# Kernel tuning notes

Measured on AMD Instinct MI355X. Metric: run time of the kernel, lower is better.

The kernel has to match this reference:

```python
import jax, jax.numpy as jnp
import numpy as np

B = 16384          # batch of graphs
N = 4              # nodes per graph (hardcoded in module)
F_IN = 4           # node features
F_E = 4            # edge features
CH = 128           # EdgeConditionedConv channels
HID = 256          # final Dense units (gnn hidden_dim)
OBS_DIM = 3 + N * F_IN + N * N + N * N * F_E  # 99


def _glorot(k, shape, fan):
    return jax.random.normal(k, shape, jnp.float32) * (1.0 / np.sqrt(fan))


def setup_inputs() -> dict:
    key = jax.random.key(0)
    ks = jax.random.split(key, 8)
    return {
        "observations": jax.random.normal(ks[0], (B, OBS_DIM), jnp.float32),
        # ECCConv filter-generating network: single Dense(F_E -> CH*F_IN)
        "W_fgn": _glorot(ks[1], (F_E, CH * F_IN), F_E),
        "b_fgn": jnp.zeros((CH * F_IN,), jnp.float32),
        # ECCConv root weight + bias
        "W_root": _glorot(ks[2], (F_IN, CH), F_IN),
        "b_conv": jnp.zeros((CH,), jnp.float32),
        # GlobalAttnSumPool attention vector
        "attn_kernel": _glorot(ks[3], (CH,), CH),
        # final Dense(tanh)
        "W_dense": _glorot(ks[4], (CH, HID), CH),
        "b_dense": jnp.zeros((HID,), jnp.float32),
    }


def reference(observations, W_fgn, b_fgn, W_root, b_conv, attn_kernel, W_dense, b_dense):
    Bn = observations.shape[0]
    obs = observations[:, 3:]
    X = obs[:, : N * F_IN].reshape(Bn, N, F_IN)                     # [B,N,F]
    A = obs[:, N * F_IN : N * F_IN + N * N].reshape(Bn, N, N)        # [B,N,N]
    E = obs[:, N * F_IN + N * N :].reshape(Bn, N, N, F_E)            # [B,N,N,Fe]

    # EdgeConditionedConv: per-edge filter generated from edge features,
    # reshaped to (B, N, N, CH, F_IN)  [channels-out first, as in spektral]
    K = (E @ W_fgn + b_fgn).reshape(Bn, N, N, CH, F_IN)
    # out[b,t,c] = sum_{s,f} A[b,t,s] * K[b,t,s,c,f] * X[b,s,f]  + root + bias
    msg = jnp.einsum('btscf,bts,bsf->btc', K, A, X)
    Xc = jax.nn.relu(msg + X @ W_root + b_conv)                      # [B,N,CH]

    # GlobalAttnSumPool: softmax over nodes of X @ a, weighted sum
    attn = jax.nn.softmax(jnp.einsum('bnc,c->bn', Xc, attn_kernel), axis=-1)
    pooled = jnp.einsum('bn,bnc->bc', attn, Xc)                      # [B,CH]

    return jnp.tanh(pooled @ W_dense + b_dense)                      # [B,HID]
```

## Files before the change

kernel.cpp:

```cpp
#include <hip/hip_runtime.h>

#define OBS_DIM 99
#define CH      128
#define HID     256
#define BPB     16

typedef short s8v __attribute__((ext_vector_type(8)));
typedef short s4v __attribute__((ext_vector_type(4)));
typedef float f4v __attribute__((ext_vector_type(4)));

__device__ __forceinline__ float ftanh(float x) {
    const float t = __expf(2.f * x);
    return 1.f - 2.f * __builtin_amdgcn_rcpf(t + 1.f);
}

__device__ __forceinline__ unsigned short f2bf(float f) {
    union { float f; unsigned u; } v; v.f = f;
    unsigned r = (v.u + 0x7fffu + ((v.u >> 16) & 1u)) >> 16;
    return (unsigned short)r;
}

__device__ __forceinline__ float bf2f(unsigned short u) {
    union { unsigned u; float f; } v; v.u = ((unsigned)u) << 16;
    return v.f;
}

__device__ __forceinline__ int kmap(int vb, int g, int j) {
    return vb ? (g * 4 + (j & 3) + 16 * (j >> 2)) : (g * 8 + j);
}

__device__ __forceinline__ float wbig_val(int k, int c, const float* Wf,
                                          const float* bf, const float* Wr,
                                          const float* bc) {
    if (k < 16) return Wf[(k >> 2) * 512 + c * 4 + (k & 3)];
    if (k < 20) return bf[c * 4 + (k - 16)];
    if (k < 24) return Wr[(k - 20) * CH + c];
    if (k == 24) return bc[c];
    return 0.f;
}

__global__ __launch_bounds__(256) void prepack(const float* __restrict__ W,
                                               const float* __restrict__ Wf,
                                               const float* __restrict__ bf,
                                               const float* __restrict__ Wr,
                                               const float* __restrict__ bc,
                                               unsigned short* __restrict__ ws) {
    const int gid = blockIdx.x * 256 + threadIdx.x;
    if (gid < 8192) {
        const int vb = gid >> 12, g = gid & 4095;
        const int tile = g >> 6, l = g & 63;
        const int kt = tile >> 4, nt = tile & 15;
        const int h = nt * 16 + (l & 15);
        unsigned short vh[8], vl[8];
        #pragma unroll
        for (int j = 0; j < 8; ++j) {
            const int k = kt * 32 + kmap(vb, l >> 4, j);
            const float wv = W[(size_t)k * HID + h];
            vh[j] = f2bf(wv);
            vl[j] = f2bf(wv - bf2f(vh[j]));
        }
        unsigned short* dh = ws + (size_t)vb * 65536 + (size_t)g * 8;
        *reinterpret_cast<s8v*>(dh)         = *reinterpret_cast<const s8v*>(vh);
        *reinterpret_cast<s8v*>(dh + 32768) = *reinterpret_cast<const s8v*>(vl);
    } else if (gid < 9216) {
        const int g2 = gid - 8192;
        const int vb = g2 >> 9, rest = g2 & 511;
        const int nt = rest >> 6, l = rest & 63;
        const int c = nt * 16 + (l & 15);
        unsigned short vh[8], vl[8];
        #pragma unroll
        for (int j = 0; j < 8; ++j) {
            const int k = kmap(vb, l >> 4, j);
            const float wv = wbig_val(k, c, Wf, bf, Wr, bc);
            vh[j] = f2bf(wv);
            vl[j] = f2bf(wv - bf2f(vh[j]));
        }
        unsigned short* dh = ws + 131072 + (size_t)vb * 8192 + (size_t)(nt * 64 + l) * 8;
        *reinterpret_cast<s8v*>(dh)        = *reinterpret_cast<const s8v*>(vh);
        *reinterpret_cast<s8v*>(dh + 4096) = *reinterpret_cast<const s8v*>(vl);
    }

    if (blockIdx.x == 0 && threadIdx.x < 64) {
        const int lane = threadIdx.x;
        const int g = lane >> 4;
        s8v ac, ab2, lab, ones;
        #pragma unroll
        for (int j = 0; j < 8; ++j) {
            ac[j]   = (short)f2bf((float)(kmap(0, g, j) + 1));
            ab2[j]  = (short)f2bf((float)(kmap(1, g, j) + 1));
            lab[j]  = (short)f2bf((float)(lane & 15));
            ones[j] = (short)0x3F80;
        }
        const f4v z = {0.f, 0.f, 0.f, 0.f};
        const f4v dcc = __builtin_amdgcn_mfma_f32_16x16x32_bf16(ac,  ac,  z, 0, 0, 0);
        const f4v dcb = __builtin_amdgcn_mfma_f32_16x16x32_bf16(ac,  ab2, z, 0, 0, 0);
        const f4v dbc = __builtin_amdgcn_mfma_f32_16x16x32_bf16(ab2, ac,  z, 0, 0, 0);
        const float EXP = 11440.f;
        int variant = 3;
        if      (__all(dcc[0] == EXP)) variant = 0;
        else if (__all(dcb[0] == EXP)) variant = 1;
        else if (__all(dbc[0] == EXP)) variant = 2;

        const f4v rowv = __builtin_amdgcn_mfma_f32_16x16x32_bf16(lab, ones, z, 0, 0, 0);
        const f4v colv = __builtin_amdgcn_mfma_f32_16x16x32_bf16(ones, lab, z, 0, 0, 0);
        int bi[4], hx[4];
        #pragma unroll
        for (int r = 0; r < 4; ++r) {
            int bv = (int)(rowv[r] * 0.03125f + 0.5f);
            int hv = (int)(colv[r] * 0.03125f + 0.5f);
            bi[r] = bv < 0 ? 0 : (bv > 15 ? 15 : bv);
            hx[r] = hv < 0 ? 0 : (hv > 15 ? 15 : hv);
        }
        bool gb = (bi[0] >> 2 == bi[1] >> 2) && (bi[1] >> 2 == bi[2] >> 2) &&
                  (bi[2] >> 2 == bi[3] >> 2);
        gb = gb && (((1 << (bi[0] & 3)) | (1 << (bi[1] & 3)) |
                     (1 << (bi[2] & 3)) | (1 << (bi[3] & 3))) == 0xF);
        gb = gb && (hx[0] == hx[1]) && (hx[1] == hx[2]) && (hx[2] == hx[3]);
        const int pk = bi[0] | (bi[1] << 4) | (bi[2] << 8) | (bi[3] << 12)
                     | (hx[0] << 16) | (hx[1] << 20) | (hx[2] << 24) | (hx[3] << 28);
        int bip = pk & 0xFFFF;
        bool same = true;
        #pragma unroll
        for (int st = 1; st < 16; st <<= 1)
            same = same && (bip == __shfl_xor(bip, st, 64));
        unsigned mset = 1u << hx[0];
        #pragma unroll
        for (int st = 1; st < 16; st <<= 1)
            mset |= (unsigned)__shfl_xor((int)mset, st, 64);
        gb = gb && same && (mset == 0xFFFFu);
        const int gb_all = __all(gb ? 1 : 0);

        int* pr = reinterpret_cast<int*>(ws + 147456);
        pr[lane] = pk;
        if (lane == 0) pr[64] = variant | (gb_all ? 16 : 0);
    }
}

__global__ __launch_bounds__(256, 4) void gnn_main(
    const float* __restrict__ obs,
    const float* __restrict__ W_fgn,
    const float* __restrict__ b_fgn,
    const float* __restrict__ W_root,
    const float* __restrict__ b_conv,
    const float* __restrict__ attn_k,
    const float* __restrict__ W_dense,
    const unsigned short* __restrict__ wb,
    const int* __restrict__ probe,
    const float* __restrict__ b_dense,
    float* __restrict__ out)
{
    __shared__ __align__(16) unsigned char smem[18944];
    auto feat_h  = reinterpret_cast<unsigned short (*)[40]>(smem);
    auto feat_l  = reinterpret_cast<unsigned short (*)[40]>(smem + 5120);
    auto part    = reinterpret_cast<float (*)[64]>(smem);
    auto attnl   = reinterpret_cast<float*>(smem + 1024);
    auto lobs    = reinterpret_cast<float (*)[96]>(smem + 10240);
    auto lpool_h = reinterpret_cast<unsigned short (*)[136]>(smem + 10240);
    auto lpool_l = reinterpret_cast<unsigned short (*)[136]>(smem + 14592);
    auto poolf   = reinterpret_cast<float (*)[136]>(smem + 10240);

    const int tid  = threadIdx.x;
    const int b0   = blockIdx.x * BPB;
    const int lane = tid & 63;
    const int w    = tid >> 6;

    int variant = 3, groupable = 0;
    int bi_r[4] = {0, 0, 0, 0}, hx_r[4] = {0, 0, 0, 0};
    if (probe) {
        const int pk   = probe[lane];
        const int meta = probe[64];
        variant   = meta & 7;
        groupable = (meta >> 4) & 1;
        #pragma unroll
        for (int r = 0; r < 4; ++r) {
            bi_r[r] = (pk >> (4 * r)) & 15;
            hx_r[r] = (pk >> (16 + 4 * r)) & 15;
        }
    }

    for (int i = tid; i < BPB * 96; i += 256) {
        const int bi = i / 96, col = i - bi * 96;
        lobs[bi][col] = obs[(size_t)(b0 + bi) * OBS_DIM + 3 + col];
    }
    __syncthreads();

    {
        const int bi = tid >> 4, t = (tid >> 2) & 3, e = tid & 3;
        const int row = bi * 4 + t;
        float m[4] = {0.f, 0.f, 0.f, 0.f};
        #pragma unroll
        for (int s = 0; s < 4; ++s) {
            const float ae = lobs[bi][16 + t * 4 + s] * lobs[bi][32 + (t * 4 + s) * 4 + e];
            #pragma unroll
            for (int f = 0; f < 4; ++f) m[f] = fmaf(ae, lobs[bi][s * 4 + f], m[f]);
        }
        #pragma unroll
        for (int f = 0; f < 4; ++f) {
            const unsigned short h = f2bf(m[f]);
            feat_h[row][e * 4 + f] = h;
            feat_l[row][e * 4 + f] = f2bf(m[f] - bf2f(h));
        }
    }
    if (tid < 64) {
        const int bi = tid >> 2, t = tid & 3, row = bi * 4 + t;
        #pragma unroll
        for (int f = 0; f < 4; ++f) {
            float ax = 0.f;
            #pragma unroll
            for (int s = 0; s < 4; ++s)
                ax = fmaf(lobs[bi][16 + t * 4 + s], lobs[bi][s * 4 + f], ax);
            const unsigned short h = f2bf(ax);
            feat_h[row][16 + f] = h;
            feat_l[row][16 + f] = f2bf(ax - bf2f(h));
        }
    } else if (tid < 128) {
        const int q = tid - 64;
        const int bi = q >> 2, t = q & 3, row = bi * 4 + t;
        #pragma unroll
        for (int f = 0; f < 4; ++f) {
            const float xv = lobs[bi][t * 4 + f];
            const unsigned short h = f2bf(xv);
            feat_h[row][20 + f] = h;
            feat_l[row][20 + f] = f2bf(xv - bf2f(h));
        }
        feat_h[row][24] = 0x3F80; feat_l[row][24] = 0;
        #pragma unroll
        for (int k = 25; k < 32; ++k) { feat_h[row][k] = 0; feat_l[row][k] = 0; }
    }
    __syncthreads();

    if (variant < 3 && groupable) {
        const int hx0 = hx_r[0];
        const int ib  = bi_r[0] >> 2;

        const s8v* B1h = reinterpret_cast<const s8v*>(wb + 131072 + (variant == 1 ? 8192 : 0));
        const s8v* B1l = B1h + 512;
        s8v bh1[2], bl1[2];
        float akv[2];
        #pragma unroll
        for (int ctl = 0; ctl < 2; ++ctl) {
            const int idx = (w * 2 + ctl) * 64 + lane;
            bh1[ctl] = B1h[idx]; bl1[ctl] = B1l[idx];
            akv[ctl] = attn_k[w * 32 + ctl * 16 + hx0];
        }

        float xc[4][2][4];
        float part16[16];
        #pragma unroll
        for (int i = 0; i < 16; ++i) part16[i] = 0.f;

        #pragma unroll
        for (int rt = 0; rt < 4; ++rt) {
            const int row = rt * 16 + (lane & 15);
            s8v ah, al;
            if (variant != 2) {
                ah = *reinterpret_cast<const s8v*>(&feat_h[row][(lane >> 4) * 8]);
                al = *reinterpret_cast<const s8v*>(&feat_l[row][(lane >> 4) * 8]);
            } else {
                const s4v h0 = *reinterpret_cast<const s4v*>(&feat_h[row][(lane >> 4) * 4]);
                const s4v h1 = *reinterpret_cast<const s4v*>(&feat_h[row][16 + (lane >> 4) * 4]);
                const s4v l0 = *reinterpret_cast<const s4v*>(&feat_l[row][(lane >> 4) * 4]);
                const s4v l1 = *reinterpret_cast<const s4v*>(&feat_l[row][16 + (lane >> 4) * 4]);
                ah = __builtin_shufflevector(h0, h1, 0, 1, 2, 3, 4, 5, 6, 7);
                al = __builtin_shufflevector(l0, l1, 0, 1, 2, 3, 4, 5, 6, 7);
            }
            #pragma unroll
            for (int ctl = 0; ctl < 2; ++ctl) {
                f4v acc = {0.f, 0.f, 0.f, 0.f};
                acc = __builtin_amdgcn_mfma_f32_16x16x32_bf16(al, bh1[ctl], acc, 0, 0, 0);
                acc = __builtin_amdgcn_mfma_f32_16x16x32_bf16(ah, bl1[ctl], acc, 0, 0, 0);
                acc = __builtin_amdgcn_mfma_f32_16x16x32_bf16(ah, bh1[ctl], acc, 0, 0, 0);
                #pragma unroll
                for (int r = 0; r < 4; ++r) {
                    const float v = fmaxf(acc[r], 0.f);
                    xc[rt][ctl][r] = v;
                    part16[rt * 4 + r] = fmaf(v, akv[ctl], part16[rt * 4 + r]);
                }
            }
        }

        #pragma unroll
        for (int st = 1; st < 16; st <<= 1) {
            #pragma unroll
            for (int i = 0; i < 16; ++i)
                part16[i] += __shfl_xor(part16[i], st, 64);
        }
        __syncthreads();
        if ((lane & 15) == 0) {
            #pragma unroll
            for (int rt = 0; rt < 4; ++rt)
                #pragma unroll
                for (int r = 0; r < 4; ++r)
                    part[w][rt * 16 + bi_r[r]] = part16[rt * 4 + r];
        }
        __syncthreads();

        if (tid < 64) {
            const float l = part[0][tid] + part[1][tid] + part[2][tid] + part[3][tid];
            float m1 = fmaxf(l, __shfl_xor(l, 1, 64));
            m1 = fmaxf(m1, __shfl_xor(m1, 2, 64));
            const float e = __expf(l - m1);
            float s = e + __shfl_xor(e, 1, 64);
            s += __shfl_xor(s, 2, 64);
            attnl[tid] = e * __builtin_amdgcn_rcpf(s);
        }
        __syncthreads();

        #pragma unroll
        for (int rt = 0; rt < 4; ++rt) {
            float p0 = 0.f, p1 = 0.f;
            #pragma unroll
            for (int r = 0; r < 4; ++r) {
                const float a = attnl[rt * 16 + bi_r[r]];
                p0 = fmaf(a, xc[rt][0][r], p0);
                p1 = fmaf(a, xc[rt][1][r], p1);
            }
            const int item = rt * 4 + ib;
            const int c0 = w * 32 + hx0, c1 = c0 + 16;
            const unsigned short h0 = f2bf(p0), h1 = f2bf(p1);
            lpool_h[item][c0] = h0;  lpool_l[item][c0] = f2bf(p0 - bf2f(h0));
            lpool_h[item][c1] = h1;  lpool_l[item][c1] = f2bf(p1 - bf2f(h1));
        }
        __syncthreads();

        const s8v* Bh = reinterpret_cast<const s8v*>(wb + (variant == 1 ? 65536 : 0));
        const s8v* Bl = reinterpret_cast<const s8v*>(wb + (variant == 1 ? 98304 : 32768));
        f4v acc2[4] = {f4v{0,0,0,0}, f4v{0,0,0,0}, f4v{0,0,0,0}, f4v{0,0,0,0}};
        #pragma unroll
        for (int ks = 0; ks < 4; ++ks) {
            s8v ah, al;
            if (variant != 2) {
                ah = *reinterpret_cast<const s8v*>(&lpool_h[lane & 15][ks * 32 + (lane >> 4) * 8]);
                al = *reinterpret_cast<const s8v*>(&lpool_l[lane & 15][ks * 32 + (lane >> 4) * 8]);
            } else {
                const s4v h0 = *reinterpret_cast<const s4v*>(&lpool_h[lane & 15][ks * 32 + (lane >> 4) * 4]);
                const s4v h1 = *reinterpret_cast<const s4v*>(&lpool_h[lane & 15][ks * 32 + 16 + (lane >> 4) * 4]);
                const s4v l0 = *reinterpret_cast<const s4v*>(&lpool_l[lane & 15][ks * 32 + (lane >> 4) * 4]);
                const s4v l1 = *reinterpret_cast<const s4v*>(&lpool_l[lane & 15][ks * 32 + 16 + (lane >> 4) * 4]);
                ah = __builtin_shufflevector(h0, h1, 0, 1, 2, 3, 4, 5, 6, 7);
                al = __builtin_shufflevector(l0, l1, 0, 1, 2, 3, 4, 5, 6, 7);
            }
            #pragma unroll
            for (int nt = 0; nt < 4; ++nt) {
                const int idx = (ks * 16 + w * 4 + nt) * 64 + lane;
                const s8v bh = Bh[idx], bl = Bl[idx];
                acc2[nt] = __builtin_amdgcn_mfma_f32_16x16x32_bf16(al, bh, acc2[nt], 0, 0, 0);
                acc2[nt] = __builtin_amdgcn_mfma_f32_16x16x32_bf16(ah, bl, acc2[nt], 0, 0, 0);
                acc2[nt] = __builtin_amdgcn_mfma_f32_16x16x32_bf16(ah, bh, acc2[nt], 0, 0, 0);
            }
        }
        #pragma unroll
        for (int nt = 0; nt < 4; ++nt) {
            #pragma unroll
            for (int r = 0; r < 4; ++r) {
                const int h = w * 64 + nt * 16 + hx_r[r];
                out[(size_t)(b0 + bi_r[r]) * HID + h] = ftanh(acc2[nt][r] + b_dense[h]);
            }
        }
    } else {
        #pragma unroll 1
        for (int p = 0; p < 4; ++p) {
            const int item = w * 4 + p;
            float xc2[2][4], pt[4] = {0.f, 0.f, 0.f, 0.f};
            #pragma unroll 1
            for (int ch = 0; ch < 2; ++ch) {
                const int cc = lane + ch * 64;
                #pragma unroll
                for (int t = 0; t < 4; ++t) {
                    const int row = item * 4 + t;
                    float v = 0.f;
                    #pragma unroll 5
                    for (int k = 0; k < 25; ++k) {
                        const float fv = bf2f(feat_h[row][k]) + bf2f(feat_l[row][k]);
                        v = fmaf(fv, wbig_val(k, cc, W_fgn, b_fgn, W_root, b_conv), v);
                    }
                    xc2[ch][t] = fmaxf(v, 0.f);
                    pt[t] = fmaf(xc2[ch][t], attn_k[cc], pt[t]);
                }
            }
            #pragma unroll
            for (int st = 1; st < 64; st <<= 1) {
                #pragma unroll
                for (int t = 0; t < 4; ++t) pt[t] += __shfl_xor(pt[t], st, 64);
            }
            const float mx = fmaxf(fmaxf(pt[0], pt[1]), fmaxf(pt[2], pt[3]));
            const float e0 = __expf(pt[0] - mx), e1 = __expf(pt[1] - mx);
            const float e2 = __expf(pt[2] - mx), e3 = __expf(pt[3] - mx);
            const float inv = 1.f / (e0 + e1 + e2 + e3);
            poolf[item][lane]      = (e0 * xc2[0][0] + e1 * xc2[0][1] + e2 * xc2[0][2] + e3 * xc2[0][3]) * inv;
            poolf[item][lane + 64] = (e0 * xc2[1][0] + e1 * xc2[1][1] + e2 * xc2[1][2] + e3 * xc2[1][3]) * inv;
        }
        __syncthreads();

        const int col0 = w * 64 + (lane & 15) * 4;
        const int rb   = (lane >> 4) * 4;
        float acc[4][4];
        #pragma unroll
        for (int j = 0; j < 4; ++j)
            #pragma unroll
            for (int i = 0; i < 4; ++i) acc[j][i] = 0.f;
        #pragma unroll 4
        for (int cc = 0; cc < CH; cc += 4) {
            float4 pv[4], wr[4];
            #pragma unroll
            for (int j = 0; j < 4; ++j) {
                pv[j].x = poolf[rb + j][cc];     pv[j].y = poolf[rb + j][cc + 1];
                pv[j].z = poolf[rb + j][cc + 2]; pv[j].w = poolf[rb + j][cc + 3];
            }
            #pragma unroll
            for (int k = 0; k < 4; ++k)
                wr[k] = *reinterpret_cast<const float4*>(&W_dense[(size_t)(cc + k) * HID + col0]);
            #pragma unroll
            for (int j = 0; j < 4; ++j) {
                const float pj[4] = {pv[j].x, pv[j].y, pv[j].z, pv[j].w};
                #pragma unroll
                for (int k = 0; k < 4; ++k) {
                    acc[j][0] = fmaf(pj[k], wr[k].x, acc[j][0]);
                    acc[j][1] = fmaf(pj[k], wr[k].y, acc[j][1]);
                    acc[j][2] = fmaf(pj[k], wr[k].z, acc[j][2]);
                    acc[j][3] = fmaf(pj[k], wr[k].w, acc[j][3]);
                }
            }
        }
        const float4 bd = *reinterpret_cast<const float4*>(&b_dense[col0]);
        #pragma unroll
        for (int j = 0; j < 4; ++j) {
            float4 o;
            o.x = ftanh(acc[j][0] + bd.x);
            o.y = ftanh(acc[j][1] + bd.y);
            o.z = ftanh(acc[j][2] + bd.z);
            o.w = ftanh(acc[j][3] + bd.w);
            *reinterpret_cast<float4*>(&out[(size_t)(b0 + rb + j) * HID + col0]) = o;
        }
    }
}

extern "C" void kernel_launch(void* const* d_in, const int* in_sizes, int n_in,
                              void* d_out, int out_size, void* d_ws, size_t ws_size,
                              hipStream_t stream) {
    const float* obs     = (const float*)d_in[0];
    const float* W_fgn   = (const float*)d_in[1];
    const float* b_fgn   = (const float*)d_in[2];
    const float* W_root  = (const float*)d_in[3];
    const float* b_conv  = (const float*)d_in[4];
    const float* attn_k  = (const float*)d_in[5];
    const float* W_dense = (const float*)d_in[6];
    const float* b_dense = (const float*)d_in[7];
    float* out = (float*)d_out;

    const int Bn = in_sizes[0] / OBS_DIM;
    const bool use_ws = (ws_size >= 320 * 1024) && (d_ws != nullptr);

    if (use_ws) {
        unsigned short* wb = (unsigned short*)d_ws;
        prepack<<<36, 256, 0, stream>>>(W_dense, W_fgn, b_fgn, W_root, b_conv, wb);
        gnn_main<<<Bn / BPB, 256, 0, stream>>>(obs, W_fgn, b_fgn, W_root, b_conv,
                                               attn_k, W_dense, wb,
                                               (const int*)(wb + 147456), b_dense, out);
    } else {
        gnn_main<<<Bn / BPB, 256, 0, stream>>>(obs, W_fgn, b_fgn, W_root, b_conv,
                                               attn_k, W_dense, nullptr, nullptr,
                                               b_dense, out);
    }
}
```

Before: 24.81 us.

## Double block to 512 threads, splitting channel and output tiles across eight waves

Launches 512-thread blocks with eight wavefronts. In the MFMA path each wave now handles one 16-channel tile of the conv instead of two, and two 16-column output tiles of the dense layer instead of four, so per-wave work and register use are halved. The attention partial sums are reduced across eight waves, and the scratch layout is shifted to fit eight partial rows. The fallback scalar path keeps only the first four waves active, and the extra threads add block scheduling and barrier cost.

```diff
diff --git a/kernel.cpp b/kernel.cpp
--- a/kernel.cpp
+++ b/kernel.cpp
@@ -136,7 +136,7 @@
     }
 }
 
-__global__ __launch_bounds__(256, 4) void gnn_main(
+__global__ __launch_bounds__(512, 8) void gnn_main(
     const float* __restrict__ obs,
     const float* __restrict__ W_fgn,
     const float* __restrict__ b_fgn,
@@ -153,7 +153,7 @@
     auto feat_h  = reinterpret_cast<unsigned short (*)[40]>(smem);
     auto feat_l  = reinterpret_cast<unsigned short (*)[40]>(smem + 5120);
     auto part    = reinterpret_cast<float (*)[64]>(smem);
-    auto attnl   = reinterpret_cast<float*>(smem + 1024);
+    auto attnl   = reinterpret_cast<float*>(smem + 2048);
     auto lobs    = reinterpret_cast<float (*)[96]>(smem + 10240);
     auto lpool_h = reinterpret_cast<unsigned short (*)[136]>(smem + 10240);
     auto lpool_l = reinterpret_cast<unsigned short (*)[136]>(smem + 14592);
@@ -178,13 +178,13 @@
         }
     }
 
-    for (int i = tid; i < BPB * 96; i += 256) {
+    for (int i = tid; i < BPB * 96; i += 512) {
         const int bi = i / 96, col = i - bi * 96;
         lobs[bi][col] = obs[(size_t)(b0 + bi) * OBS_DIM + 3 + col];
     }
     __syncthreads();
 
-    {
+    if (tid < 256) {
         const int bi = tid >> 4, t = (tid >> 2) & 3, e = tid & 3;
         const int row = bi * 4 + t;
         float m[4] = {0.f, 0.f, 0.f, 0.f};
@@ -200,9 +200,9 @@
             feat_h[row][e * 4 + f] = h;
             feat_l[row][e * 4 + f] = f2bf(m[f] - bf2f(h));
         }
-    }
-    if (tid < 64) {
-        const int bi = tid >> 2, t = tid & 3, row = bi * 4 + t;
+    } else if (tid < 320) {
+        const int q = tid - 256;
+        const int bi = q >> 2, t = q & 3, row = bi * 4 + t;
         #pragma unroll
         for (int f = 0; f < 4; ++f) {
             float ax = 0.f;
@@ -213,8 +213,8 @@
             feat_h[row][16 + f] = h;
             feat_l[row][16 + f] = f2bf(ax - bf2f(h));
         }
-    } else if (tid < 128) {
-        const int q = tid - 64;
+    } else if (tid < 384) {
+        const int q = tid - 320;
         const int bi = q >> 2, t = q & 3, row = bi * 4 + t;
         #pragma unroll
         for (int f = 0; f < 4; ++f) {
@@ -235,19 +235,12 @@
 
         const s8v* B1h = reinterpret_cast<const s8v*>(wb + 131072 + (variant == 1 ? 8192 : 0));
         const s8v* B1l = B1h + 512;
-        s8v bh1[2], bl1[2];
-        float akv[2];
-        #pragma unroll
-        for (int ctl = 0; ctl < 2; ++ctl) {
-            const int idx = (w * 2 + ctl) * 64 + lane;
-            bh1[ctl] = B1h[idx]; bl1[ctl] = B1l[idx];
-            akv[ctl] = attn_k[w * 32 + ctl * 16 + hx0];
-        }
-
-        float xc[4][2][4];
+        const s8v bh1 = B1h[w * 64 + lane];
+        const s8v bl1 = B1l[w * 64 + lane];
+        const float akv = attn_k[w * 16 + hx0];
+
+        float xc[4][4];
         float part16[16];
-        #pragma unroll
-        for (int i = 0; i < 16; ++i) part16[i] = 0.f;
 
         #pragma unroll
         for (int rt = 0; rt < 4; ++rt) {
@@ -264,18 +257,15 @@
                 ah = __builtin_shufflevector(h0, h1, 0, 1, 2, 3, 4, 5, 6, 7);
                 al = __builtin_shufflevector(l0, l1, 0, 1, 2, 3, 4, 5, 6, 7);
             }
-            #pragma unroll
-            for (int ctl = 0; ctl < 2; ++ctl) {
-                f4v acc = {0.f, 0.f, 0.f, 0.f};
-                acc = __builtin_amdgcn_mfma_f32_16x16x32_bf16(al, bh1[ctl], acc, 0, 0, 0);
-                acc = __builtin_amdgcn_mfma_f32_16x16x32_bf16(ah, bl1[ctl], acc, 0, 0, 0);
-                acc = __builtin_amdgcn_mfma_f32_16x16x32_bf16(ah, bh1[ctl], acc, 0, 0, 0);
-                #pragma unroll
-                for (int r = 0; r < 4; ++r) {
-                    const float v = fmaxf(acc[r], 0.f);
-                    xc[rt][ctl][r] = v;
-                    part16[rt * 4 + r] = fmaf(v, akv[ctl], part16[rt * 4 + r]);
-                }
+            f4v acc = {0.f, 0.f, 0.f, 0.f};
+            acc = __builtin_amdgcn_mfma_f32_16x16x32_bf16(al, bh1, acc, 0, 0, 0);
+            acc = __builtin_amdgcn_mfma_f32_16x16x32_bf16(ah, bl1, acc, 0, 0, 0);
+            acc = __builtin_amdgcn_mfma_f32_16x16x32_bf16(ah, bh1, acc, 0, 0, 0);
+            #pragma unroll
+            for (int r = 0; r < 4; ++r) {
+                const float v = fmaxf(acc[r], 0.f);
+                xc[rt][r] = v;
+                part16[rt * 4 + r] = v * akv;
             }
         }
 
@@ -296,7 +286,9 @@
         __syncthreads();
 
         if (tid < 64) {
-            const float l = part[0][tid] + part[1][tid] + part[2][tid] + part[3][tid];
+            float l = 0.f;
+            #pragma unroll
+            for (int q = 0; q < 8; ++q) l += part[q][tid];
             float m1 = fmaxf(l, __shfl_xor(l, 1, 64));
             m1 = fmaxf(m1, __shfl_xor(m1, 2, 64));
             const float e = __expf(l - m1);
@@ -308,25 +300,22 @@
 
         #pragma unroll
         for (int rt = 0; rt < 4; ++rt) {
-            float p0 = 0.f, p1 = 0.f;
-            #pragma unroll
-            for (int r = 0; r < 4; ++r) {
-                const float a = attnl[rt * 16 + bi_r[r]];
-                p0 = fmaf(a, xc[rt][0][r], p0);
-                p1 = fmaf(a, xc[rt][1][r], p1);
-            }
+            float p = 0.f;
+            #pragma unroll
+            for (int r = 0; r < 4; ++r)
+                p = fmaf(attnl[rt * 16 + bi_r[r]], xc[rt][r], p);
             const int item = rt * 4 + ib;
-            const int c0 = w * 32 + hx0, c1 = c0 + 16;
-            const unsigned short h0 = f2bf(p0), h1 = f2bf(p1);
-            lpool_h[item][c0] = h0;  lpool_l[item][c0] = f2bf(p0 - bf2f(h0));
-            lpool_h[item][c1] = h1;  lpool_l[item][c1] = f2bf(p1 - bf2f(h1));
+            const int c = w * 16 + hx0;
+            const unsigned short h = f2bf(p);
+            lpool_h[item][c] = h;
+            lpool_l[item][c] = f2bf(p - bf2f(h));
         }
         __syncthreads();
 
         const s8v* Bh = reinterpret_cast<const s8v*>(wb + (variant == 1 ? 65536 : 0));
         const s8v* Bl = reinterpret_cast<const s8v*>(wb + (variant == 1 ? 98304 : 32768));
-        f4v acc2[4] = {f4v{0,0,0,0}, f4v{0,0,0,0}, f4v{0,0,0,0}, f4v{0,0,0,0}};
-        #pragma unroll
+        f4v acc2[2] = {f4v{0,0,0,0}, f4v{0,0,0,0}};
+        #pragma unroll 1
         for (int ks = 0; ks < 4; ++ks) {
             s8v ah, al;
             if (variant != 2) {
@@ -341,96 +330,100 @@
                 al = __builtin_shufflevector(l0, l1, 0, 1, 2, 3, 4, 5, 6, 7);
             }
             #pragma unroll
-            for (int nt = 0; nt < 4; ++nt) {
-                const int idx = (ks * 16 + w * 4 + nt) * 64 + lane;
+            for (int ntl = 0; ntl < 2; ++ntl) {
+                const int idx = (ks * 16 + (w * 2 + ntl)) * 64 + lane;
                 const s8v bh = Bh[idx], bl = Bl[idx];
-                acc2[nt] = __builtin_amdgcn_mfma_f32_16x16x32_bf16(al, bh, acc2[nt], 0, 0, 0);
-                acc2[nt] = __builtin_amdgcn_mfma_f32_16x16x32_bf16(ah, bl, acc2[nt], 0, 0, 0);
-                acc2[nt] = __builtin_amdgcn_mfma_f32_16x16x32_bf16(ah, bh, acc2[nt], 0, 0, 0);
-            }
-        }
-        #pragma unroll
-        for (int nt = 0; nt < 4; ++nt) {
+                acc2[ntl] = __builtin_amdgcn_mfma_f32_16x16x32_bf16(al, bh, acc2[ntl], 0, 0, 0);
+                acc2[ntl] = __builtin_amdgcn_mfma_f32_16x16x32_bf16(ah, bl, acc2[ntl], 0, 0, 0);
+                acc2[ntl] = __builtin_amdgcn_mfma_f32_16x16x32_bf16(ah, bh, acc2[ntl], 0, 0, 0);
+            }
+        }
+        #pragma unroll
+        for (int ntl = 0; ntl < 2; ++ntl) {
             #pragma unroll
             for (int r = 0; r < 4; ++r) {
-                const int h = w * 64 + nt * 16 + hx_r[r];
-                out[(size_t)(b0 + bi_r[r]) * HID + h] = ftanh(acc2[nt][r] + b_dense[h]);
+                const int h = (w * 2 + ntl) * 16 + hx_r[r];
+                out[(size_t)(b0 + bi_r[r]) * HID + h] = ftanh(acc2[ntl][r] + b_dense[h]);
             }
         }
     } else {
-        #pragma unroll 1
-        for (int p = 0; p < 4; ++p) {
-            const int item = w * 4 + p;
-            float xc2[2][4], pt[4] = {0.f, 0.f, 0.f, 0.f};
+        if (w < 4) {
             #pragma unroll 1
-            for (int ch = 0; ch < 2; ++ch) {
-                const int cc = lane + ch * 64;
-                #pragma unroll
-                for (int t = 0; t < 4; ++t) {
-                    const int row = item * 4 + t;
-                    float v = 0.f;
-                    #pragma unroll 5
-                    for (int k = 0; k < 25; ++k) {
-                        const float fv = bf2f(feat_h[row][k]) + bf2f(feat_l[row][k]);
-                        v = fmaf(fv, wbig_val(k, cc, W_fgn, b_fgn, W_root, b_conv), v);
+            for (int p = 0; p < 4; ++p) {
+                const int item = w * 4 + p;
+                float xc2[2][4], pt[4] = {0.f, 0.f, 0.f, 0.f};
+                #pragma unroll 1
+                for (int ch = 0; ch < 2; ++ch) {
+                    const int cc = lane + ch * 64;
+                    #pragma unroll
+                    for (int t = 0; t < 4; ++t) {
+                        const int row = item * 4 + t;
+                        float v = 0.f;
+                        #pragma unroll 5
+                        for (int k = 0; k < 25; ++k) {
+                            const float fv = bf2f(feat_h[row][k]) + bf2f(feat_l[row][k]);
+                            v = fmaf(fv, wbig_val(k, cc, W_fgn, b_fgn, W_root, b_conv), v);
+                        }
+                        xc2[ch][t] = fmaxf(v, 0.f);
+                        pt[t] = fmaf(xc2[ch][t], attn_k[cc], pt[t]);
                     }
-                    xc2[ch][t] = fmaxf(v, 0.f);
-                    pt[t] = fmaf(xc2[ch][t], attn_k[cc], pt[t]);
                 }
-            }
-            #pragma unroll
-            for (int st = 1; st < 64; st <<= 1) {
-                #pragma unroll
-                for (int t = 0; t < 4; ++t) pt[t] += __shfl_xor(pt[t], st, 64);
-            }
-            const float mx = fmaxf(fmaxf(pt[0], pt[1]), fmaxf(pt[2], pt[3]));
-            const float e0 = __expf(pt[0] - mx), e1 = __expf(pt[1] - mx);
-            const float e2 = __expf(pt[2] - mx), e3 = __expf(pt[3] - mx);
-            const float inv = 1.f / (e0 + e1 + e2 + e3);
-            poolf[item][lane]      = (e0 * xc2[0][0] + e1 * xc2[0][1] + e2 * xc2[0][2] + e3 * xc2[0][3]) * inv;
-            poolf[item][lane + 64] = (e0 * xc2[1][0] + e1 * xc2[1][1] + e2 * xc2[1][2] + e3 * xc2[1][3]) * inv;
+                #pragma unroll
+                for (int st = 1; st < 64; st <<= 1) {
+                    #pragma unroll
+                    for (int t = 0; t < 4; ++t) pt[t] += __shfl_xor(pt[t], st, 64);
+                }
+                const float mx = fmaxf(fmaxf(pt[0], pt[1]), fmaxf(pt[2], pt[3]));
+                const float e0 = __expf(pt[0] - mx), e1 = __expf(pt[1] - mx);
+                const float e2 = __expf(pt[2] - mx), e3 = __expf(pt[3] - mx);
+                const float inv = 1.f / (e0 + e1 + e2 + e3);
+                poolf[item][lane]      = (e0 * xc2[0][0] + e1 * xc2[0][1] + e2 * xc2[0][2] + e3 * xc2[0][3]) * inv;
+                poolf[item][lane + 64] = (e0 * xc2[1][0] + e1 * xc2[1][1] + e2 * xc2[1][2] + e3 * xc2[1][3]) * inv;
+            }
         }
         __syncthreads();
 
-        const int col0 = w * 64 + (lane & 15) * 4;
-        const int rb   = (lane >> 4) * 4;
-        float acc[4][4];
-        #pragma unroll
-        for (int j = 0; j < 4; ++j)
-            #pragma unroll
-            for (int i = 0; i < 4; ++i) acc[j][i] = 0.f;
-        #pragma unroll 4
-        for (int cc = 0; cc < CH; cc += 4) {
-            float4 pv[4], wr[4];
+        if (w < 4) {
+            const int col0 = w * 64 + (lane & 15) * 4;
+            const int rb   = (lane >> 4) * 4;
+            float acc[4][4];
+            #pragma unroll
+            for (int j = 0; j < 4; ++j)
+                #pragma unroll
+                for (int i = 0; i < 4; ++i) acc[j][i] = 0.f;
+            #pragma unroll 4
+            for (int cc = 0; cc < CH; cc += 4) {
+                float4 pv[4], wr[4];
+                #pragma unroll
+                for (int j = 0; j < 4; ++j) {
+                    pv[j].x = poolf[rb + j][cc];     pv[j].y = poolf[rb + j][cc + 1];
+                    pv[j].z = poolf[rb + j][cc + 2]; pv[j].w = poolf[rb + j][cc + 3];
+                }
+                #pragma unroll
+                for (int k = 0; k < 4; ++k)
+                    wr[k] = *reinterpret_cast<const float4*>(&W_dense[(size_t)(cc + k) * HID + col0]);
+                #pragma unroll
+                for (int j = 0; j < 4; ++j) {
+                    const float pj[4] = {pv[j].x, pv[j].y, pv[j].z, pv[j].w};
+                    #pragma unroll
+                    for (int k = 0; k < 4; ++k) {
+                        acc[j][0] = fmaf(pj[k], wr[k].x, acc[j][0]);
+                        acc[j][1] = fmaf(pj[k], wr[k].y, acc[j][1]);
+                        acc[j][2] = fmaf(pj[k], wr[k].z, acc[j][2]);
+                        acc[j][3] = fmaf(pj[k], wr[k].w, acc[j][3]);
+                    }
+                }
+            }
+            const float4 bd = *reinterpret_cast<const float4*>(&b_dense[col0]);
             #pragma unroll
             for (int j = 0; j < 4; ++j) {
-                pv[j].x = poolf[rb + j][cc];     pv[j].y = poolf[rb + j][cc + 1];
-                pv[j].z = poolf[rb + j][cc + 2]; pv[j].w = poolf[rb + j][cc + 3];
-            }
-            #pragma unroll
-            for (int k = 0; k < 4; ++k)
-                wr[k] = *reinterpret_cast<const float4*>(&W_dense[(size_t)(cc + k) * HID + col0]);
-            #pragma unroll
-            for (int j = 0; j < 4; ++j) {
-                const float pj[4] = {pv[j].x, pv[j].y, pv[j].z, pv[j].w};
-                #pragma unroll
-                for (int k = 0; k < 4; ++k) {
-                    acc[j][0] = fmaf(pj[k], wr[k].x, acc[j][0]);
-                    acc[j][1] = fmaf(pj[k], wr[k].y, acc[j][1]);
-                    acc[j][2] = fmaf(pj[k], wr[k].z, acc[j][2]);
-                    acc[j][3] = fmaf(pj[k], wr[k].w, acc[j][3]);
-                }
-            }
-        }
-        const float4 bd = *reinterpret_cast<const float4*>(&b_dense[col0]);
-        #pragma unroll
-        for (int j = 0; j < 4; ++j) {
-            float4 o;
-            o.x = ftanh(acc[j][0] + bd.x);
-            o.y = ftanh(acc[j][1] + bd.y);
-            o.z = ftanh(acc[j][2] + bd.z);
-            o.w = ftanh(acc[j][3] + bd.w);
-            *reinterpret_cast<float4*>(&out[(size_t)(b0 + rb + j) * HID + col0]) = o;
+                float4 o;
+                o.x = ftanh(acc[j][0] + bd.x);
+                o.y = ftanh(acc[j][1] + bd.y);
+                o.z = ftanh(acc[j][2] + bd.z);
+                o.w = ftanh(acc[j][3] + bd.w);
+                *reinterpret_cast<float4*>(&out[(size_t)(b0 + rb + j) * HID + col0]) = o;
+            }
         }
     }
 }
@@ -454,11 +447,11 @@
     if (use_ws) {
         unsigned short* wb = (unsigned short*)d_ws;
         prepack<<<36, 256, 0, stream>>>(W_dense, W_fgn, b_fgn, W_root, b_conv, wb);
-        gnn_main<<<Bn / BPB, 256, 0, stream>>>(obs, W_fgn, b_fgn, W_root, b_conv,
+        gnn_main<<<Bn / BPB, 512, 0, stream>>>(obs, W_fgn, b_fgn, W_root, b_conv,
                                                attn_k, W_dense, wb,
                                                (const int*)(wb + 147456), b_dense, out);
     } else {
-        gnn_main<<<Bn / BPB, 256, 0, stream>>>(obs, W_fgn, b_fgn, W_root, b_conv,
+        gnn_main<<<Bn / BPB, 512, 0, stream>>>(obs, W_fgn, b_fgn, W_root, b_conv,
                                                attn_k, W_dense, nullptr, nullptr,
                                                b_dense, out);
     }
```

After: 27.22 us. 9.7% more time.
